# Performance work log

Measured on AMD Instinct MI355X. Metric: run time of the kernel, lower is better.

## Reference

```python
import jax, jax.numpy as jnp
import numpy as np
from jax import lax

SCOPE = 15
RICKER_WIDTH = 3.0
DAMP = 0.12
MAX_STEPS = 10


def mexican_hat(scope, width, damping):
    # ricker / mexican-hat wavelet sampled at `scope` integer-spaced points, scaled by damping
    x = np.linspace(-(scope // 2), scope // 2, scope).astype(np.float32)
    norm = 2.0 / (np.sqrt(3.0 * width) * np.pi ** 0.25)
    w = damping * norm * (1.0 - (x / width) ** 2) * np.exp(-(x ** 2) / (2.0 * width ** 2))
    return jnp.asarray(w, dtype=jnp.float32)


def setup_inputs() -> dict:
    key = jax.random.key(0)
    activations = jax.random.normal(key, (32, 256, 56, 56), dtype=jnp.float32)
    w_rec = mexican_hat(SCOPE, RICKER_WIDTH, DAMP)  # [scope]
    return {"activations": activations, "w_rec": w_rec, "max_steps": MAX_STEPS}


def reference(activations, w_rec, max_steps):
    # activations: [B, C, H, W]; inhibition conv runs along the C axis only.
    scope = w_rec.shape[0]
    pad = scope // 2
    x = activations[:, None]                     # [B, 1, C, H, W]
    kernel = w_rec.reshape(1, 1, scope, 1, 1)    # OIDHW

    def conv(y):
        return lax.conv_general_dilated(
            y, kernel,
            window_strides=(1, 1, 1),
            padding=[(pad, pad), (0, 0), (0, 0)],
            dimension_numbers=("NCDHW", "OIDHW", "NCDHW"),
        )

    # fixed-point iteration: state <- activations + W_rec * state  (threshold=0 => always max_steps iters)
    state = x
    for _ in range(max_steps):
        state = x + conv(state)
    return state[:, 0]  # squeeze channel dim -> [B, C, H, W]
```

## Files before the change

kernel.cpp:

```cpp
#include <hip/hip_runtime.h>


#define NCH 256
#define PAD 7
#define SCOPE 15
#define SPATIAL 3136
#define PER_B 802816
#define STW 32
#define STILES_PER_B 98
#define NTILES 3136
#define MAXCH 12

typedef __attribute__((ext_vector_type(8))) __bf16 bf16x8;
typedef __attribute__((ext_vector_type(16))) float float16;
typedef __attribute__((ext_vector_type(4))) unsigned int uint4v;
typedef __attribute__((ext_vector_type(2))) unsigned int uint2v;

static __device__ __forceinline__ unsigned short f2bf_rn_u(float f) {
  unsigned u = __builtin_bit_cast(unsigned int, f);
  return (unsigned short)((u + 0x7FFFu + ((u >> 16) & 1u)) >> 16);
}
static __device__ __forceinline__ float bf2f_u(unsigned short h) {
  unsigned u = ((unsigned)h) << 16;
  return __builtin_bit_cast(float, u);
}
static __device__ __forceinline__ unsigned pack_bf2(float a, float b) {
  return (unsigned)f2bf_rn_u(a) | ((unsigned)f2bf_rn_u(b) << 16);
}
static __device__ __forceinline__ void split2(float a, float b,
                                              unsigned& h, unsigned& l) {
  h = pack_bf2(a, b);
  const float ra = a - __builtin_bit_cast(float, h << 16);
  const float rb = b - __builtin_bit_cast(float, h & 0xFFFF0000u);
  l = pack_bf2(ra, rb);
}

__global__ void build_M_kernel(const float* __restrict__ w,
                               const int* __restrict__ max_steps_p,
                               unsigned short* __restrict__ AhF,
                               unsigned short* __restrict__ AlF) {
  const int d = blockIdx.x;
  const int c = threadIdx.x;
  __shared__ float v[2][NCH];
  __shared__ float wsh[SCOPE];
  if (c < SCOPE) wsh[c] = w[c];
  const float e = (c == d) ? 1.0f : 0.0f;
  v[0][c] = e;
  __syncthreads();
  const int steps = *max_steps_p;
  int cur = 0;
  for (int t = 0; t < steps; ++t) {
    float s = e;
#pragma unroll
    for (int j = 0; j < SCOPE; ++j) {
      const int cc = c + j - PAD;
      if (cc >= 0 && cc < NCH) s += wsh[j] * v[cur][cc];
    }
    cur ^= 1;
    v[cur][c] = s;
    __syncthreads();
  }
  const float f = v[cur][c];
  const unsigned short h = f2bf_rn_u(f);
  const unsigned short l = f2bf_rn_u(f - bf2f_u(h));

  const int wv = c >> 5;
  const int c0 = wv * 32;
  int clo = c0 - 70; if (clo < 0) clo = 0; clo >>= 4;
  int chi = c0 + 101; if (chi > 255) chi = 255; chi >>= 4;
  const int ch = d >> 4;
  if (ch >= clo && ch <= chi) {
    const int i    = ch - clo;
    const int half = (d >> 3) & 1;
    const int j    = d & 7;
    const int lane = half * 32 + (c & 31);
    const size_t dst = ((size_t)(wv * MAXCH + i) * 64 + lane) * 8 + j;
    AhF[dst] = h;
    AlF[dst] = l;
  }
}


#define LOADA(dh, dl, i)                                   \
  {                                                        \
    dh = *(const bf16x8*)(mhp + (i) * 512);                \
    dl = *(const bf16x8*)(mlp + (i) * 512);                \
  }
#define LOADA_P(dh, dl, i)                                 \
  if ((i) < nch) LOADA(dh, dl, i)

#define CHUNK(Ahr, Alr, i)                                              \
  {                                                                     \
    const int k2b = (clo + (i)) * 8 + half * 4;                         \
    const unsigned* bp = &XB[k2b * 64 + 2 * m];                         \
    const uint2v r0 = *(const uint2v*)(bp);                             \
    const uint2v r1 = *(const uint2v*)(bp + 64);                        \
    const uint2v r2 = *(const uint2v*)(bp + 128);                       \
    const uint2v r3 = *(const uint2v*)(bp + 192);                       \
    const uint4v hw = {r0.x, r1.x, r2.x, r3.x};                         \
    const uint4v lw = {r0.y, r1.y, r2.y, r3.y};                         \
    const bf16x8 bh = __builtin_bit_cast(bf16x8, hw);                   \
    const bf16x8 bl = __builtin_bit_cast(bf16x8, lw);                   \
    acc = __builtin_amdgcn_mfma_f32_32x32x16_bf16(Ahr, bh, acc, 0, 0, 0); \
    acc = __builtin_amdgcn_mfma_f32_32x32x16_bf16(Ahr, bl, acc, 0, 0, 0); \
    acc = __builtin_amdgcn_mfma_f32_32x32x16_bf16(Alr, bh, acc, 0, 0, 0); \
  }
#define CHUNK_P(Ahr, Alr, i)                               \
  if ((i) < nch) CHUNK(Ahr, Alr, i)

__global__ __launch_bounds__(512, 6) void apply_M_kernel(
    const float* __restrict__ x, const unsigned short* __restrict__ AhF,
    const unsigned short* __restrict__ AlF, float* __restrict__ out) {
  __shared__ unsigned XB[8192];

  const int tid  = threadIdx.x;
  const int lane = tid & 63;
  const int w    = tid >> 6;
  const int m    = lane & 31;
  const int half = lane >> 5;
  const int c0   = w * 32;

  int clo = c0 - 70; if (clo < 0) clo = 0; clo >>= 4;
  int chi = c0 + 101; if (chi > 255) chi = 255; chi >>= 4;
  const int nch = chi - clo + 1;

  const int sq = (tid & 7) * 4;
  const int dg = tid >> 3;

  const int tau = blockIdx.x;
  const float* gb = x + (size_t)(tau / STILES_PER_B) * PER_B
                      + (size_t)(tau % STILES_PER_B) * STW;
  const float4 g0 = *(const float4*)(gb + (size_t)(2 * dg) * SPATIAL + sq);
  const float4 g1 = *(const float4*)(gb + (size_t)(2 * dg + 1) * SPATIAL + sq);
  const float4 g2 = *(const float4*)(gb + (size_t)(2 * dg + 128) * SPATIAL + sq);
  const float4 g3 = *(const float4*)(gb + (size_t)(2 * dg + 129) * SPATIAL + sq);

  const unsigned short* mhp = AhF + ((size_t)(w * MAXCH) * 64 + lane) * 8;
  const unsigned short* mlp = AlF + ((size_t)(w * MAXCH) * 64 + lane) * 8;

  bf16x8 pH0, pL0, pH1, pL1, pH2, pL2;
  bf16x8 qH0, qL0, qH1, qL1, qH2, qL2;
  LOADA(pH0, pL0, 0) LOADA(pH1, pL1, 1) LOADA(pH2, pL2, 2)

  {
    unsigned h0, h1, h2, h3, l0, l1, l2, l3;
    split2(g0.x, g1.x, h0, l0); split2(g0.y, g1.y, h1, l1);
    split2(g0.z, g1.z, h2, l2); split2(g0.w, g1.w, h3, l3);
    unsigned* p = &XB[dg * 64 + sq * 2];
    *(uint4v*)(p)     = (uint4v){h0, l0, h1, l1};
    *(uint4v*)(p + 4) = (uint4v){h2, l2, h3, l3};
    split2(g2.x, g3.x, h0, l0); split2(g2.y, g3.y, h1, l1);
    split2(g2.z, g3.z, h2, l2); split2(g2.w, g3.w, h3, l3);
    unsigned* q = &XB[(dg + 64) * 64 + sq * 2];
    *(uint4v*)(q)     = (uint4v){h0, l0, h1, l1};
    *(uint4v*)(q + 4) = (uint4v){h2, l2, h3, l3};
  }

  asm volatile("s_waitcnt lgkmcnt(0)" ::: "memory");
  __builtin_amdgcn_s_barrier();

  float16 acc;
#pragma unroll
  for (int q = 0; q < 16; ++q) acc[q] = 0.0f;

  LOADA(qH0, qL0, 3) LOADA(qH1, qL1, 4) LOADA(qH2, qL2, 5)
  CHUNK(pH0, pL0, 0) CHUNK(pH1, pL1, 1) CHUNK(pH2, pL2, 2)

  LOADA(pH0, pL0, 6) LOADA_P(pH1, pL1, 7) LOADA_P(pH2, pL2, 8)
  CHUNK(qH0, qL0, 3) CHUNK(qH1, qL1, 4) CHUNK(qH2, qL2, 5)

  LOADA_P(qH0, qL0, 9) LOADA_P(qH1, qL1, 10) LOADA_P(qH2, qL2, 11)
  CHUNK(pH0, pL0, 6) CHUNK_P(pH1, pL1, 7) CHUNK_P(pH2, pL2, 8)

  CHUNK_P(qH0, qL0, 9) CHUNK_P(qH1, qL1, 10) CHUNK_P(qH2, qL2, 11)

  const int b  = tau / STILES_PER_B;
  const int s0 = (tau % STILES_PER_B) * STW;
  float* ob = out + (size_t)b * PER_B + (size_t)s0 + m;
#pragma unroll
  for (int r = 0; r < 16; ++r) {
    const int row = (r & 3) + 8 * (r >> 2) + 4 * half;
    ob[(size_t)(c0 + row) * SPATIAL] = acc[r];
  }
}

extern "C" void kernel_launch(void* const* d_in, const int* in_sizes, int n_in,
                              void* d_out, int out_size, void* d_ws, size_t ws_size,
                              hipStream_t stream) {
  const float* x = (const float*)d_in[0];
  const float* w = (const float*)d_in[1];
  const int* ms = (const int*)d_in[2];
  float* out = (float*)d_out;

  unsigned short* AhF = (unsigned short*)d_ws;
  unsigned short* AlF = AhF + 8 * MAXCH * 64 * 8;

  build_M_kernel<<<NCH, NCH, 0, stream>>>(w, ms, AhF, AlF);
  apply_M_kernel<<<NTILES, 512, 0, stream>>>(x, AhF, AlF, out);
}
```

Baseline: 230.4 us.

## Widen spatial tile to 64 columns with two accumulators per wave

Doubles the spatial tile per block from 32 to 64 columns. Each wave now keeps two MFMA accumulators, so every A-matrix (M) fragment loaded from global memory is reused across two B tiles, and the block count is halved. It also makes the A loads unconditional and inserts sched_barriers to pin load and MFMA ordering. In exchange it uses twice the LDS per block, more registers, and a lower occupancy hint in launch_bounds (4 instead of 6).

```diff
diff --git a/kernel.cpp b/kernel.cpp
--- a/kernel.cpp
+++ b/kernel.cpp
@@ -6,9 +6,9 @@
 #define SCOPE 15
 #define SPATIAL 3136
 #define PER_B 802816
-#define STW 32
-#define STILES_PER_B 98
-#define NTILES 3136
+#define STW 64
+#define STILES_PER_B 49
+#define NTILES 1568
 #define MAXCH 12
 
 typedef __attribute__((ext_vector_type(8))) __bf16 bf16x8;
@@ -86,32 +86,42 @@
     dh = *(const bf16x8*)(mhp + (i) * 512);                \
     dl = *(const bf16x8*)(mlp + (i) * 512);                \
   }
-#define LOADA_P(dh, dl, i)                                 \
-  if ((i) < nch) LOADA(dh, dl, i)
-
-#define CHUNK(Ahr, Alr, i)                                              \
-  {                                                                     \
-    const int k2b = (clo + (i)) * 8 + half * 4;                         \
-    const unsigned* bp = &XB[k2b * 64 + 2 * m];                         \
-    const uint2v r0 = *(const uint2v*)(bp);                             \
-    const uint2v r1 = *(const uint2v*)(bp + 64);                        \
-    const uint2v r2 = *(const uint2v*)(bp + 128);                       \
-    const uint2v r3 = *(const uint2v*)(bp + 192);                       \
-    const uint4v hw = {r0.x, r1.x, r2.x, r3.x};                         \
-    const uint4v lw = {r0.y, r1.y, r2.y, r3.y};                         \
-    const bf16x8 bh = __builtin_bit_cast(bf16x8, hw);                   \
-    const bf16x8 bl = __builtin_bit_cast(bf16x8, lw);                   \
-    acc = __builtin_amdgcn_mfma_f32_32x32x16_bf16(Ahr, bh, acc, 0, 0, 0); \
-    acc = __builtin_amdgcn_mfma_f32_32x32x16_bf16(Ahr, bl, acc, 0, 0, 0); \
-    acc = __builtin_amdgcn_mfma_f32_32x32x16_bf16(Alr, bh, acc, 0, 0, 0); \
+
+#define CHUNK(Ahr, Alr, i)                                                \
+  {                                                                       \
+    const int k2b = (clo + (i)) * 8 + half * 4;                           \
+    const unsigned* bp = &XB[k2b * 128 + 2 * m];                          \
+    const uint2v r0 = *(const uint2v*)(bp);                               \
+    const uint2v r1 = *(const uint2v*)(bp + 128);                         \
+    const uint2v r2 = *(const uint2v*)(bp + 256);                         \
+    const uint2v r3 = *(const uint2v*)(bp + 384);                         \
+    const unsigned* bq = bp + 64;                                         \
+    const uint2v s0v = *(const uint2v*)(bq);                              \
+    const uint2v s1v = *(const uint2v*)(bq + 128);                        \
+    const uint2v s2v = *(const uint2v*)(bq + 256);                        \
+    const uint2v s3v = *(const uint2v*)(bq + 384);                        \
+    const bf16x8 bh0 = __builtin_bit_cast(bf16x8,                         \
+        (uint4v){r0.x, r1.x, r2.x, r3.x});                                \
+    const bf16x8 bl0 = __builtin_bit_cast(bf16x8,                         \
+        (uint4v){r0.y, r1.y, r2.y, r3.y});                                \
+    const bf16x8 bh1 = __builtin_bit_cast(bf16x8,                         \
+        (uint4v){s0v.x, s1v.x, s2v.x, s3v.x});                            \
+    const bf16x8 bl1 = __builtin_bit_cast(bf16x8,                         \
+        (uint4v){s0v.y, s1v.y, s2v.y, s3v.y});                            \
+    acc0 = __builtin_amdgcn_mfma_f32_32x32x16_bf16(Ahr, bh0, acc0, 0, 0, 0); \
+    acc1 = __builtin_amdgcn_mfma_f32_32x32x16_bf16(Ahr, bh1, acc1, 0, 0, 0); \
+    acc0 = __builtin_amdgcn_mfma_f32_32x32x16_bf16(Ahr, bl0, acc0, 0, 0, 0); \
+    acc1 = __builtin_amdgcn_mfma_f32_32x32x16_bf16(Ahr, bl1, acc1, 0, 0, 0); \
+    acc0 = __builtin_amdgcn_mfma_f32_32x32x16_bf16(Alr, bh0, acc0, 0, 0, 0); \
+    acc1 = __builtin_amdgcn_mfma_f32_32x32x16_bf16(Alr, bh1, acc1, 0, 0, 0); \
   }
 #define CHUNK_P(Ahr, Alr, i)                               \
   if ((i) < nch) CHUNK(Ahr, Alr, i)
 
-__global__ __launch_bounds__(512, 6) void apply_M_kernel(
+__global__ __launch_bounds__(512, 4) void apply_M_kernel(
     const float* __restrict__ x, const unsigned short* __restrict__ AhF,
     const unsigned short* __restrict__ AlF, float* __restrict__ out) {
-  __shared__ unsigned XB[8192];
+  __shared__ unsigned XB[16384];
 
   const int tid  = threadIdx.x;
   const int lane = tid & 63;
@@ -124,16 +134,20 @@
   int chi = c0 + 101; if (chi > 255) chi = 255; chi >>= 4;
   const int nch = chi - clo + 1;
 
-  const int sq = (tid & 7) * 4;
-  const int dg = tid >> 3;
+  const int sq = (tid & 15) * 4;
+  const int dg = tid >> 4;
 
   const int tau = blockIdx.x;
   const float* gb = x + (size_t)(tau / STILES_PER_B) * PER_B
                       + (size_t)(tau % STILES_PER_B) * STW;
   const float4 g0 = *(const float4*)(gb + (size_t)(2 * dg) * SPATIAL + sq);
   const float4 g1 = *(const float4*)(gb + (size_t)(2 * dg + 1) * SPATIAL + sq);
-  const float4 g2 = *(const float4*)(gb + (size_t)(2 * dg + 128) * SPATIAL + sq);
-  const float4 g3 = *(const float4*)(gb + (size_t)(2 * dg + 129) * SPATIAL + sq);
+  const float4 g2 = *(const float4*)(gb + (size_t)(2 * dg + 64) * SPATIAL + sq);
+  const float4 g3 = *(const float4*)(gb + (size_t)(2 * dg + 65) * SPATIAL + sq);
+  const float4 g4 = *(const float4*)(gb + (size_t)(2 * dg + 128) * SPATIAL + sq);
+  const float4 g5 = *(const float4*)(gb + (size_t)(2 * dg + 129) * SPATIAL + sq);
+  const float4 g6 = *(const float4*)(gb + (size_t)(2 * dg + 192) * SPATIAL + sq);
+  const float4 g7 = *(const float4*)(gb + (size_t)(2 * dg + 193) * SPATIAL + sq);
 
   const unsigned short* mhp = AhF + ((size_t)(w * MAXCH) * 64 + lane) * 8;
   const unsigned short* mlp = AlF + ((size_t)(w * MAXCH) * 64 + lane) * 8;
@@ -141,35 +155,49 @@
   bf16x8 pH0, pL0, pH1, pL1, pH2, pL2;
   bf16x8 qH0, qL0, qH1, qL1, qH2, qL2;
   LOADA(pH0, pL0, 0) LOADA(pH1, pL1, 1) LOADA(pH2, pL2, 2)
+  __builtin_amdgcn_sched_barrier(0);
 
   {
     unsigned h0, h1, h2, h3, l0, l1, l2, l3;
     split2(g0.x, g1.x, h0, l0); split2(g0.y, g1.y, h1, l1);
     split2(g0.z, g1.z, h2, l2); split2(g0.w, g1.w, h3, l3);
-    unsigned* p = &XB[dg * 64 + sq * 2];
+    unsigned* p = &XB[dg * 128 + sq * 2];
     *(uint4v*)(p)     = (uint4v){h0, l0, h1, l1};
     *(uint4v*)(p + 4) = (uint4v){h2, l2, h3, l3};
     split2(g2.x, g3.x, h0, l0); split2(g2.y, g3.y, h1, l1);
     split2(g2.z, g3.z, h2, l2); split2(g2.w, g3.w, h3, l3);
-    unsigned* q = &XB[(dg + 64) * 64 + sq * 2];
-    *(uint4v*)(q)     = (uint4v){h0, l0, h1, l1};
-    *(uint4v*)(q + 4) = (uint4v){h2, l2, h3, l3};
+    p = &XB[(dg + 32) * 128 + sq * 2];
+    *(uint4v*)(p)     = (uint4v){h0, l0, h1, l1};
+    *(uint4v*)(p + 4) = (uint4v){h2, l2, h3, l3};
+    split2(g4.x, g5.x, h0, l0); split2(g4.y, g5.y, h1, l1);
+    split2(g4.z, g5.z, h2, l2); split2(g4.w, g5.w, h3, l3);
+    p = &XB[(dg + 64) * 128 + sq * 2];
+    *(uint4v*)(p)     = (uint4v){h0, l0, h1, l1};
+    *(uint4v*)(p + 4) = (uint4v){h2, l2, h3, l3};
+    split2(g6.x, g7.x, h0, l0); split2(g6.y, g7.y, h1, l1);
+    split2(g6.z, g7.z, h2, l2); split2(g6.w, g7.w, h3, l3);
+    p = &XB[(dg + 96) * 128 + sq * 2];
+    *(uint4v*)(p)     = (uint4v){h0, l0, h1, l1};
+    *(uint4v*)(p + 4) = (uint4v){h2, l2, h3, l3};
   }
 
   asm volatile("s_waitcnt lgkmcnt(0)" ::: "memory");
   __builtin_amdgcn_s_barrier();
 
-  float16 acc;
+  float16 acc0, acc1;
 #pragma unroll
-  for (int q = 0; q < 16; ++q) acc[q] = 0.0f;
+  for (int q = 0; q < 16; ++q) { acc0[q] = 0.0f; acc1[q] = 0.0f; }
 
   LOADA(qH0, qL0, 3) LOADA(qH1, qL1, 4) LOADA(qH2, qL2, 5)
+  __builtin_amdgcn_sched_barrier(0);
   CHUNK(pH0, pL0, 0) CHUNK(pH1, pL1, 1) CHUNK(pH2, pL2, 2)
 
-  LOADA(pH0, pL0, 6) LOADA_P(pH1, pL1, 7) LOADA_P(pH2, pL2, 8)
+  LOADA(pH0, pL0, 6) LOADA(pH1, pL1, 7) LOADA(pH2, pL2, 8)
+  __builtin_amdgcn_sched_barrier(0);
   CHUNK(qH0, qL0, 3) CHUNK(qH1, qL1, 4) CHUNK(qH2, qL2, 5)
 
-  LOADA_P(qH0, qL0, 9) LOADA_P(qH1, qL1, 10) LOADA_P(qH2, qL2, 11)
+  LOADA(qH0, qL0, 9) LOADA(qH1, qL1, 10) LOADA(qH2, qL2, 11)
+  __builtin_amdgcn_sched_barrier(0);
   CHUNK(pH0, pL0, 6) CHUNK_P(pH1, pL1, 7) CHUNK_P(pH2, pL2, 8)
 
   CHUNK_P(qH0, qL0, 9) CHUNK_P(qH1, qL1, 10) CHUNK_P(qH2, qL2, 11)
@@ -180,7 +208,9 @@
 #pragma unroll
   for (int r = 0; r < 16; ++r) {
     const int row = (r & 3) + 8 * (r >> 2) + 4 * half;
-    ob[(size_t)(c0 + row) * SPATIAL] = acc[r];
+    float* orow = ob + (size_t)(c0 + row) * SPATIAL;
+    orow[0]  = acc0[r];
+    orow[32] = acc1[r];
   }
 }
 
```

New measurement: 205.6 us. 10.8% less time.
